# Optimization experiments

Hardware: AMD Instinct MI355X
Metric: run time of the kernel (lower is better)

Reference implementation:

```python
import jax, jax.numpy as jnp
import numpy as np

N_HEADS = 8
EMBED_C = 256  # key/query channels
OUT_C = 256    # value/output channels
MASK_CENTER = True

def setup_inputs() -> dict:
    key = jax.random.key(0)
    ks = jax.random.split(key, 5)
    B, C, H, W = 32, 256, 32, 32
    x = jax.random.normal(ks[0], (B, C, H, W), dtype=jnp.float32)
    # 1x1 conv weights as [out, in] matrices; scaled like torch conv default init
    s = 1.0 / np.sqrt(C)
    q_w = jax.random.normal(ks[1], (EMBED_C, C), dtype=jnp.float32) * s
    q_b = jax.random.normal(ks[2], (EMBED_C,), dtype=jnp.float32) * s
    kv_w = jax.random.normal(ks[3], (EMBED_C + OUT_C, C), dtype=jnp.float32) * s
    kv_b = jax.random.normal(ks[4], (EMBED_C + OUT_C,), dtype=jnp.float32) * s
    return {"x": x, "q_w": q_w, "q_b": q_b, "kv_w": kv_w, "kv_b": kv_b}

def _to_multihead(t):
    # t: (B, C, S) -> (B, n_heads, S, C // n_heads)
    B, C, S = t.shape
    return jnp.transpose(t.reshape(B, N_HEADS, C // N_HEADS, S), (0, 1, 3, 2))

def reference(x, q_w, q_b, kv_w, kv_b):
    B, C, H, W = x.shape
    S = H * W
    xf = x.reshape(B, C, S)  # flatten spatial; 1x1 conv == channel matmul
    q = jnp.einsum('oc,bcs->bos', q_w, xf) + q_b[None, :, None]
    kv = jnp.einsum('oc,bcs->bos', kv_w, xf) + kv_b[None, :, None]
    k, v = kv[:, :EMBED_C], kv[:, EMBED_C:]
    q = _to_multihead(q)   # (B, h, S, dk)
    k = _to_multihead(k)   # (B, h, S, dk)
    v = _to_multihead(v)   # (B, h, S, dv)
    dk = k.shape[-1]
    # strictly-lower-triangular causal mask (center pixel masked)
    mask = jnp.tril(jnp.ones((S, S), dtype=x.dtype), -int(MASK_CENTER))
    scores = jnp.einsum('bhqd,bhkd->bhqk', q, k) / jnp.sqrt(jnp.asarray(dk, x.dtype))
    scores = jnp.where(mask == 0, jnp.asarray(-10000.0, x.dtype), scores)
    attn = jax.nn.softmax(scores, axis=-1)
    attn = jnp.where(mask == 0, jnp.asarray(0.0, x.dtype), attn)
    out = jnp.einsum('bhqk,bhkd->bhqd', attn, v)  # (B, h, S, dv)
    out = jnp.transpose(out, (0, 1, 3, 2)).reshape(B, OUT_C, H, W)
    return out
```

## Files before the change

kernel.cpp:

```cpp
#include <hip/hip_runtime.h>
#include <hip/hip_bf16.h>

typedef __attribute__((ext_vector_type(8))) short short8;
typedef __attribute__((ext_vector_type(4))) float f32x4;
typedef __attribute__((ext_vector_type(16))) float f32x16;

#define B_  32
#define CH  256
#define S_  1024
#define NH  8
#define HD  32

static __device__ __forceinline__ unsigned short f2bf(float f) {
  __hip_bfloat16 h = __float2bfloat16(f);
  return *reinterpret_cast<unsigned short*>(&h);
}

static __device__ __forceinline__ void gl_lds16(const void* g, void* l) {
  __builtin_amdgcn_global_load_lds(
      (const __attribute__((address_space(1))) void*)g,
      (__attribute__((address_space(3))) void*)l, 16, 0, 0);
}

__global__ void k_prep(const float* __restrict__ x, unsigned short* __restrict__ xt,
                       const float* __restrict__ qw, const float* __restrict__ qb,
                       const float* __restrict__ kvw, const float* __restrict__ kvb,
                       unsigned short* __restrict__ wt, float* __restrict__ bias) {
  __shared__ float tile[32][33];
  int blk = (int)blockIdx.x;
  int t = threadIdx.x;
  if (blk < 8192) {
    int b = blk >> 8;
    int inner = blk & 255;
    int ct = inner >> 5, st = inner & 31;
    int c0 = ct * 32, s0 = st * 32;
    int r = t >> 3, q4 = (t & 7) * 4;
    const float4 v = *reinterpret_cast<const float4*>(
        x + ((size_t)(b * CH + c0 + r)) * S_ + s0 + q4);
    tile[r][q4 + 0] = v.x; tile[r][q4 + 1] = v.y;
    tile[r][q4 + 2] = v.z; tile[r][q4 + 3] = v.w;
    __syncthreads();
    ushort4 u;
    u.x = f2bf(tile[q4 + 0][r]); u.y = f2bf(tile[q4 + 1][r]);
    u.z = f2bf(tile[q4 + 2][r]); u.w = f2bf(tile[q4 + 3][r]);
    *reinterpret_cast<ushort4*>(xt + ((size_t)(b * S_ + s0 + r)) * CH + c0 + q4) = u;
  } else {
    int gid = (blk - 8192) * 256 + t;
    const float rs = 0.25503531838951954f;
    int o = gid >> 8, c = gid & 255;
    float v = (o < 256) ? qw[o * 256 + c] * rs : kvw[(o - 256) * 256 + c];
    wt[gid] = f2bf(v);
    if (gid < 768) bias[gid] = (gid < 256) ? qb[gid] * rs : kvb[gid - 256];
  }
}

__global__ __launch_bounds__(512) void k_proj(
    const unsigned short* __restrict__ wt, const float* __restrict__ bias,
    const unsigned short* __restrict__ xt,
    unsigned short* __restrict__ qws, unsigned short* __restrict__ kv) {
  __shared__ __align__(16) union {
    struct { unsigned short As[2][4096]; unsigned short Bs[2][4096]; } g;
    unsigned short vst[16384];
  } SH;
  int b = blockIdx.y;
  int mt = blockIdx.x >> 3, nt = blockIdx.x & 7;
  int tid = threadIdx.x;
  int wid = tid >> 6, l = tid & 63;
  int rb = l >> 4, lr = l & 15;
  int wr = wid >> 2, wc = wid & 3;
  int mb = mt * 128, nb = nt * 128;
  int wm = wr * 64, wn = wc * 32;
  const unsigned short* xb = xt + (size_t)b * S_ * CH;

  int r0 = tid >> 2, k0 = (tid & 3) * 8;
  const unsigned short* wa0 = wt + (size_t)(mb + r0) * CH + k0;
  const unsigned short* xb0 = xb + (size_t)(nb + r0) * CH + k0;
  char* asb = (char*)&SH.g.As[0][0];
  char* bsb = (char*)&SH.g.Bs[0][0];
  int wb = wid * 1024;

  f32x4 acc[4][2];
  #pragma unroll
  for (int mf = 0; mf < 4; ++mf)
    #pragma unroll
    for (int nf = 0; nf < 2; ++nf)
      acc[mf][nf] = (f32x4){0.f, 0.f, 0.f, 0.f};

  gl_lds16(wa0, asb + wb);
  gl_lds16(xb0, bsb + wb);
  __syncthreads();

  #pragma unroll 1
  for (int kk = 0; kk < 8; ++kk) {
    int cur = kk & 1;
    bool more = (kk < 7);
    if (more) {
      int ko = (kk + 1) * 32;
      int bo = (cur ^ 1) * 8192 + wb;
      gl_lds16(wa0 + ko, asb + bo);
      gl_lds16(xb0 + ko, bsb + bo);
    }

    short8 a[4], bfr[2];
    #pragma unroll
    for (int mf = 0; mf < 4; ++mf)
      a[mf] = *reinterpret_cast<const short8*>(
          &SH.g.As[cur][(wm + mf * 16 + lr) * 32 + rb * 8]);
    #pragma unroll
    for (int nf = 0; nf < 2; ++nf)
      bfr[nf] = *reinterpret_cast<const short8*>(
          &SH.g.Bs[cur][(wn + nf * 16 + lr) * 32 + rb * 8]);
    #pragma unroll
    for (int mf = 0; mf < 4; ++mf)
      #pragma unroll
      for (int nf = 0; nf < 2; ++nf)
        acc[mf][nf] = __builtin_amdgcn_mfma_f32_16x16x32_bf16(
            a[mf], bfr[nf], acc[mf][nf], 0, 0, 0);

    __syncthreads();
  }

  if (mb < 256) {
    #pragma unroll
    for (int mf = 0; mf < 4; ++mf) {
      int m0 = mb + wm + mf * 16 + rb * 4;
      const float4 bv = *reinterpret_cast<const float4*>(bias + m0);
      #pragma unroll
      for (int nf = 0; nf < 2; ++nf) {
        int n = nb + wn + nf * 16 + lr;
        ushort4 u = {f2bf(acc[mf][nf][0] + bv.x), f2bf(acc[mf][nf][1] + bv.y),
                     f2bf(acc[mf][nf][2] + bv.z), f2bf(acc[mf][nf][3] + bv.w)};
        int h = m0 >> 5, d = m0 & 31;
        *reinterpret_cast<ushort4*>(
            qws + ((size_t)(b * NH + h) * S_ + n) * HD + d) = u;
      }
    }
  } else {
    const bool isV = (mb >= 512);
    const int voff = isV ? 1024 : 0;
    unsigned short* vst = SH.vst;
    #pragma unroll
    for (int mf = 0; mf < 4; ++mf) {
      int m0 = mb + wm + mf * 16 + rb * 4;
      const float4 bv = *reinterpret_cast<const float4*>(bias + m0);
      int mml = wm + mf * 16 + rb * 4;
      int hl = mml >> 5, d0 = mml & 31;
      #pragma unroll
      for (int nf = 0; nf < 2; ++nf) {
        int nlc = wn + nf * 16 + lr;
        int tl = nlc >> 5, nl = nlc & 31;
        float v0 = acc[mf][nf][0] + bv.x;
        float v1 = acc[mf][nf][1] + bv.y;
        float v2 = acc[mf][nf][2] + bv.z;
        float v3 = acc[mf][nf][3] + bv.w;
        int tb = (hl * 4 + tl) * 1024;
        if (isV) {
          int kp = (nl & 19) | (((nl >> 2) & 1) << 3) | (((nl >> 3) & 1) << 2);
          int base = tb + (kp >> 3) * 256 + (kp & 7);
          vst[base + (size_t)(d0 + 0) * 8] = f2bf(v0);
          vst[base + (size_t)(d0 + 1) * 8] = f2bf(v1);
          vst[base + (size_t)(d0 + 2) * 8] = f2bf(v2);
          vst[base + (size_t)(d0 + 3) * 8] = f2bf(v3);
        } else {
          ushort4 u = {f2bf(v0), f2bf(v1), f2bf(v2), f2bf(v3)};
          *reinterpret_cast<ushort4*>(
              &vst[tb + (d0 >> 3) * 256 + nl * 8 + (d0 & 7)]) = u;
        }
      }
    }
    __syncthreads();
    int tt = tid >> 5, j = tid & 31;
    int hb = (isV ? (mb - 512) : (mb - 256)) >> 5;
    int h = hb + (tt >> 2);
    size_t gb = ((size_t)(b * NH + h) * 32 + (nt * 4 + (tt & 3))) * 2048 + voff;
    #pragma unroll
    for (int s = 0; s < 4; ++s) {
      int off = (j + s * 32) * 8;
      *reinterpret_cast<short8*>(kv + gb + off) =
          *reinterpret_cast<const short8*>(vst + tt * 1024 + off);
    }
  }
}

__global__ __launch_bounds__(512, 4) void k_attn(
    const unsigned short* __restrict__ qws, const unsigned short* __restrict__ kv,
    float* __restrict__ out) {
  __shared__ __align__(16) unsigned short kvbuf[2][8192];
  int tid = threadIdx.x;
  int wid = tid >> 6, l = tid & 63;
  int col = l & 31, hi = l >> 5;
  int bh = (int)(blockIdx.x & 255);
  int g  = 3 - (int)(blockIdx.x >> 8);
  int qt = g * 8 + wid;
  int q0 = qt << 5;
  int niter = g * 2 + 2;

  const unsigned short* Q   = qws + (size_t)bh * S_ * HD;
  const unsigned short* kvb = kv + (size_t)bh * 32 * 2048;
  char* kb0 = (char*)&kvbuf[0][0];
  int wb = wid * 1024;

  short8 aq0 = *reinterpret_cast<const short8*>(Q + (q0 + col) * HD + hi * 8);
  short8 aq1 = *reinterpret_cast<const short8*>(Q + (q0 + col) * HD + 16 + hi * 8);

  f32x16 z, O;
  #pragma unroll
  for (int i = 0; i < 16; ++i) { z[i] = 0.f; O[i] = 0.f; }
  float lsA = 0.f, lsB = 0.f;

  gl_lds16(kvb + tid * 8,        kb0 + wb);
  gl_lds16(kvb + 4096 + tid * 8, kb0 + 8192 + wb);
  __syncthreads();

  #pragma unroll 1
  for (int i = 0; i < niter; ++i) {
    int cur = i & 1;
    bool more = (i + 1 < niter);
    if (more) {
      const unsigned short* src = kvb + (size_t)(i + 1) * 8192 + tid * 8;
      char* dst = kb0 + (cur ^ 1) * 16384 + wb;
      gl_lds16(src,        dst);
      gl_lds16(src + 4096, dst + 8192);
    }

    #pragma unroll
    for (int sub = 0; sub < 4; ++sub) {
      int t = 4 * i + sub;
      if (qt >= t) {
        const unsigned short* Kb = &kvbuf[cur][sub * 2048];
        short8 bk0 = *reinterpret_cast<const short8*>(Kb + hi * 256 + col * 8);
        short8 bk1 = *reinterpret_cast<const short8*>(Kb + 512 + hi * 256 + col * 8);
        short8 av0 = *reinterpret_cast<const short8*>(Kb + 1024 + hi * 256 + col * 8);
        short8 av1 = *reinterpret_cast<const short8*>(Kb + 1536 + hi * 256 + col * 8);

        f32x16 st = __builtin_amdgcn_mfma_f32_32x32x16_bf16(bk0, aq0, z, 0, 0, 0);
        st = __builtin_amdgcn_mfma_f32_32x32x16_bf16(bk1, aq1, st, 0, 0, 0);

        float p[16];
        if (t == qt) {
          #pragma unroll
          for (int r = 0; r < 16; ++r) {
            int key = (r & 3) + 8 * (r >> 2) + 4 * hi;
            float e = __builtin_amdgcn_exp2f(st[r]);
            p[r] = (key < col) ? e : 0.f;
          }
        } else {
          #pragma unroll
          for (int r = 0; r < 16; ++r) p[r] = __builtin_amdgcn_exp2f(st[r]);
        }

        lsA += ((p[0] + p[1]) + (p[2] + p[3])) + ((p[4] + p[5]) + (p[6] + p[7]));
        lsB += ((p[8] + p[9]) + (p[10] + p[11])) + ((p[12] + p[13]) + (p[14] + p[15]));

        union { unsigned int u[8]; short8 v[2]; } pb;
        #pragma unroll
        for (int jj = 0; jj < 8; ++jj)
          asm("v_cvt_pk_bf16_f32 %0, %1, %2"
              : "=v"(pb.u[jj]) : "v"(p[2 * jj]), "v"(p[2 * jj + 1]));

        O = __builtin_amdgcn_mfma_f32_32x32x16_bf16(av0, pb.v[0], O, 0, 0, 0);
        O = __builtin_amdgcn_mfma_f32_32x32x16_bf16(av1, pb.v[1], O, 0, 0, 0);
      }
    }

    __syncthreads();
  }

  float lsum = lsA + lsB;
  float ltot = lsum + __shfl_xor(lsum, 32);
  float linv = (ltot > 0.f) ? 1.f / ltot : 0.f;
  int b = bh >> 3, h = bh & 7;
  float* ob = out + ((size_t)(b * 256 + h * 32)) * S_ + q0 + col;
  #pragma unroll
  for (int r = 0; r < 16; ++r) {
    int d = (r & 3) + 8 * (r >> 2) + 4 * hi;
    ob[(size_t)d * S_] = O[r] * linv;
  }
}

extern "C" void kernel_launch(void* const* d_in, const int* in_sizes, int n_in,
                              void* d_out, int out_size, void* d_ws, size_t ws_size,
                              hipStream_t stream) {
  const float* x   = (const float*)d_in[0];
  const float* qw  = (const float*)d_in[1];
  const float* qb  = (const float*)d_in[2];
  const float* kvw = (const float*)d_in[3];
  const float* kvb = (const float*)d_in[4];
  float* out = (float*)d_out;

  char* ws = (char*)d_ws;
  unsigned short* wt   = (unsigned short*)(ws + 0);
  float*          bias = (float*)(ws + 393216);
  unsigned short* xt   = (unsigned short*)(ws + 396288);
  unsigned short* qws  = (unsigned short*)(ws + 17173504);
  unsigned short* kv   = (unsigned short*)(ws + 33950720);

  k_prep<<<8960, 256, 0, stream>>>(x, xt, qw, qb, kvw, kvb, wt, bias);
  k_proj<<<dim3(48, 32), 512, 0, stream>>>(wt, bias, xt, qws, kv);
  k_attn<<<1024, 512, 0, stream>>>(qws, kv, out);
}
```

Before: 68.45 us.

## Triple-buffer projection GEMM with explicit vmcnt waits and one barrier per step

Replaces the double-buffered K loop in the projection kernel with a fully unrolled three-stage pipeline. Global-to-LDS loads are issued two steps ahead and gated with explicit s_waitcnt vmcnt counts, so each step needs one barrier instead of the trailing __syncthreads. A barrier is added before the epilogue reuses shared memory. This aims to hide global load latency in a short K loop, at the cost of more LDS and fragile hand-written wait and barrier ordering.

```diff
diff --git a/kernel.cpp b/kernel.cpp
--- a/kernel.cpp
+++ b/kernel.cpp
@@ -54,12 +54,43 @@
   }
 }
 
+
+#define VMW(n) asm volatile("s_waitcnt vmcnt(" #n ")" ::: "memory")
+#define SBAR() do { __builtin_amdgcn_s_barrier(); \
+                    __builtin_amdgcn_sched_barrier(0); } while (0)
+#define LGKM0() do { asm volatile("s_waitcnt lgkmcnt(0)" ::: "memory"); \
+                     __builtin_amdgcn_sched_barrier(0); } while (0)
+
+#define PROJ_ISSUE(step, buf) do {                                  \
+    gl_lds16(wa0 + (step) * 32, asb + (buf) * 8192 + wb);           \
+    gl_lds16(xb0 + (step) * 32, bsb + (buf) * 8192 + wb);           \
+  } while (0)
+
+#define PROJ_COMPUTE(buf) do {                                      \
+    short8 a[4], bfr[2];                                            \
+    _Pragma("unroll")                                               \
+    for (int mf = 0; mf < 4; ++mf)                                  \
+      a[mf] = *reinterpret_cast<const short8*>(                     \
+          &SH.g.As[buf][(wm + mf * 16 + lr) * 32 + rb * 8]);        \
+    _Pragma("unroll")                                               \
+    for (int nf = 0; nf < 2; ++nf)                                  \
+      bfr[nf] = *reinterpret_cast<const short8*>(                   \
+          &SH.g.Bs[buf][(wn + nf * 16 + lr) * 32 + rb * 8]);        \
+    LGKM0();                                                        \
+    _Pragma("unroll")                                               \
+    for (int mf = 0; mf < 4; ++mf)                                  \
+      _Pragma("unroll")                                             \
+      for (int nf = 0; nf < 2; ++nf)                                \
+        acc[mf][nf] = __builtin_amdgcn_mfma_f32_16x16x32_bf16(      \
+            a[mf], bfr[nf], acc[mf][nf], 0, 0, 0);                  \
+  } while (0)
+
 __global__ __launch_bounds__(512) void k_proj(
     const unsigned short* __restrict__ wt, const float* __restrict__ bias,
     const unsigned short* __restrict__ xt,
     unsigned short* __restrict__ qws, unsigned short* __restrict__ kv) {
   __shared__ __align__(16) union {
-    struct { unsigned short As[2][4096]; unsigned short Bs[2][4096]; } g;
+    struct { unsigned short As[3][4096]; unsigned short Bs[3][4096]; } g;
     unsigned short vst[16384];
   } SH;
   int b = blockIdx.y;
@@ -86,39 +117,16 @@
     for (int nf = 0; nf < 2; ++nf)
       acc[mf][nf] = (f32x4){0.f, 0.f, 0.f, 0.f};
 
-  gl_lds16(wa0, asb + wb);
-  gl_lds16(xb0, bsb + wb);
-  __syncthreads();
-
-  #pragma unroll 1
-  for (int kk = 0; kk < 8; ++kk) {
-    int cur = kk & 1;
-    bool more = (kk < 7);
-    if (more) {
-      int ko = (kk + 1) * 32;
-      int bo = (cur ^ 1) * 8192 + wb;
-      gl_lds16(wa0 + ko, asb + bo);
-      gl_lds16(xb0 + ko, bsb + bo);
-    }
-
-    short8 a[4], bfr[2];
-    #pragma unroll
-    for (int mf = 0; mf < 4; ++mf)
-      a[mf] = *reinterpret_cast<const short8*>(
-          &SH.g.As[cur][(wm + mf * 16 + lr) * 32 + rb * 8]);
-    #pragma unroll
-    for (int nf = 0; nf < 2; ++nf)
-      bfr[nf] = *reinterpret_cast<const short8*>(
-          &SH.g.Bs[cur][(wn + nf * 16 + lr) * 32 + rb * 8]);
-    #pragma unroll
-    for (int mf = 0; mf < 4; ++mf)
-      #pragma unroll
-      for (int nf = 0; nf < 2; ++nf)
-        acc[mf][nf] = __builtin_amdgcn_mfma_f32_16x16x32_bf16(
-            a[mf], bfr[nf], acc[mf][nf], 0, 0, 0);
-
-    __syncthreads();
-  }
+  PROJ_ISSUE(0, 0); PROJ_ISSUE(1, 1);
+
+  VMW(2); SBAR(); PROJ_ISSUE(2, 2); PROJ_COMPUTE(0);
+  VMW(2); SBAR(); PROJ_ISSUE(3, 0); PROJ_COMPUTE(1);
+  VMW(2); SBAR(); PROJ_ISSUE(4, 1); PROJ_COMPUTE(2);
+  VMW(2); SBAR(); PROJ_ISSUE(5, 2); PROJ_COMPUTE(0);
+  VMW(2); SBAR(); PROJ_ISSUE(6, 0); PROJ_COMPUTE(1);
+  VMW(2); SBAR(); PROJ_ISSUE(7, 1); PROJ_COMPUTE(2);
+  VMW(2); SBAR();                   PROJ_COMPUTE(0);
+  VMW(0); SBAR();                   PROJ_COMPUTE(1);
 
   if (mb < 256) {
     #pragma unroll
@@ -136,6 +144,7 @@
       }
     }
   } else {
+    __syncthreads();
     const bool isV = (mb >= 512);
     const int voff = isV ? 1024 : 0;
     unsigned short* vst = SH.vst;
```

New measurement: 67.84 us (median of 2 runs). No clear change (-0.9%).

## Fuse x transpose and bf16 conversion into projection GEMM loads

Applied to the files above, without the earlier changes.

Removes the separate pass that transposed x and converted it to bf16 in a workspace. The projection kernel now streams fp32 x tiles directly into LDS in channel-major layout and converts each element to bf16 while building the MFMA B fragments. This saves one full read and write of the activation tensor and a kernel launch. In exchange, global reads of x in the GEMM double in bytes, each tile is re-read by the six M-tiles, and B fragments are now built from scalar strided LDS reads plus per-element conversion.

```diff
diff --git a/kernel.cpp b/kernel.cpp
--- a/kernel.cpp
+++ b/kernel.cpp
@@ -22,44 +22,26 @@
       (__attribute__((address_space(3))) void*)l, 16, 0, 0);
 }
 
-__global__ void k_prep(const float* __restrict__ x, unsigned short* __restrict__ xt,
-                       const float* __restrict__ qw, const float* __restrict__ qb,
-                       const float* __restrict__ kvw, const float* __restrict__ kvb,
-                       unsigned short* __restrict__ wt, float* __restrict__ bias) {
-  __shared__ float tile[32][33];
-  int blk = (int)blockIdx.x;
-  int t = threadIdx.x;
-  if (blk < 8192) {
-    int b = blk >> 8;
-    int inner = blk & 255;
-    int ct = inner >> 5, st = inner & 31;
-    int c0 = ct * 32, s0 = st * 32;
-    int r = t >> 3, q4 = (t & 7) * 4;
-    const float4 v = *reinterpret_cast<const float4*>(
-        x + ((size_t)(b * CH + c0 + r)) * S_ + s0 + q4);
-    tile[r][q4 + 0] = v.x; tile[r][q4 + 1] = v.y;
-    tile[r][q4 + 2] = v.z; tile[r][q4 + 3] = v.w;
-    __syncthreads();
-    ushort4 u;
-    u.x = f2bf(tile[q4 + 0][r]); u.y = f2bf(tile[q4 + 1][r]);
-    u.z = f2bf(tile[q4 + 2][r]); u.w = f2bf(tile[q4 + 3][r]);
-    *reinterpret_cast<ushort4*>(xt + ((size_t)(b * S_ + s0 + r)) * CH + c0 + q4) = u;
-  } else {
-    int gid = (blk - 8192) * 256 + t;
-    const float rs = 0.25503531838951954f;
-    int o = gid >> 8, c = gid & 255;
-    float v = (o < 256) ? qw[o * 256 + c] * rs : kvw[(o - 256) * 256 + c];
-    wt[gid] = f2bf(v);
-    if (gid < 768) bias[gid] = (gid < 256) ? qb[gid] * rs : kvb[gid - 256];
-  }
+__global__ void k_wconv(const float* __restrict__ qw, const float* __restrict__ qb,
+                        const float* __restrict__ kvw, const float* __restrict__ kvb,
+                        unsigned short* __restrict__ wt, float* __restrict__ bias) {
+  int gid = (int)blockIdx.x * 256 + threadIdx.x;
+  const float rs = 0.25503531838951954f;
+  int o = gid >> 8, c = gid & 255;
+  float v = (o < 256) ? qw[o * 256 + c] * rs : kvw[(o - 256) * 256 + c];
+  wt[gid] = f2bf(v);
+  if (gid < 768) bias[gid] = (gid < 256) ? qb[gid] * rs : kvb[gid - 256];
 }
 
 __global__ __launch_bounds__(512) void k_proj(
     const unsigned short* __restrict__ wt, const float* __restrict__ bias,
-    const unsigned short* __restrict__ xt,
+    const float* __restrict__ x,
     unsigned short* __restrict__ qws, unsigned short* __restrict__ kv) {
   __shared__ __align__(16) union {
-    struct { unsigned short As[2][4096]; unsigned short Bs[2][4096]; } g;
+    struct {
+      unsigned short As[2][4096];
+      float Bf[2][4096];
+    } g;
     unsigned short vst[16384];
   } SH;
   int b = blockIdx.y;
@@ -70,13 +52,12 @@
   int wr = wid >> 2, wc = wid & 3;
   int mb = mt * 128, nb = nt * 128;
   int wm = wr * 64, wn = wc * 32;
-  const unsigned short* xb = xt + (size_t)b * S_ * CH;
-
-  int r0 = tid >> 2, k0 = (tid & 3) * 8;
-  const unsigned short* wa0 = wt + (size_t)(mb + r0) * CH + k0;
-  const unsigned short* xb0 = xb + (size_t)(nb + r0) * CH + k0;
+
+  const unsigned short* wa0 = wt + (size_t)(mb + (tid >> 2)) * CH + (tid & 3) * 8;
+  const float* xsrc = x + (size_t)b * CH * S_
+                    + (size_t)(tid >> 5) * S_ + nb + (tid & 31) * 4;
   char* asb = (char*)&SH.g.As[0][0];
-  char* bsb = (char*)&SH.g.Bs[0][0];
+  char* bfb = (char*)&SH.g.Bf[0][0];
   int wb = wid * 1024;
 
   f32x4 acc[4][2];
@@ -87,18 +68,19 @@
       acc[mf][nf] = (f32x4){0.f, 0.f, 0.f, 0.f};
 
   gl_lds16(wa0, asb + wb);
-  gl_lds16(xb0, bsb + wb);
+  gl_lds16(xsrc,             bfb + wb);
+  gl_lds16(xsrc + 16 * S_,   bfb + 8192 + wb);
   __syncthreads();
 
   #pragma unroll 1
   for (int kk = 0; kk < 8; ++kk) {
     int cur = kk & 1;
-    bool more = (kk < 7);
-    if (more) {
+    if (kk < 7) {
       int ko = (kk + 1) * 32;
-      int bo = (cur ^ 1) * 8192 + wb;
-      gl_lds16(wa0 + ko, asb + bo);
-      gl_lds16(xb0 + ko, bsb + bo);
+      gl_lds16(wa0 + ko, asb + (cur ^ 1) * 8192 + wb);
+      const float* xs = xsrc + (size_t)ko * S_;
+      gl_lds16(xs,           bfb + (cur ^ 1) * 16384 + wb);
+      gl_lds16(xs + 16 * S_, bfb + (cur ^ 1) * 16384 + 8192 + wb);
     }
 
     short8 a[4], bfr[2];
@@ -107,9 +89,12 @@
       a[mf] = *reinterpret_cast<const short8*>(
           &SH.g.As[cur][(wm + mf * 16 + lr) * 32 + rb * 8]);
     #pragma unroll
-    for (int nf = 0; nf < 2; ++nf)
-      bfr[nf] = *reinterpret_cast<const short8*>(
-          &SH.g.Bs[cur][(wn + nf * 16 + lr) * 32 + rb * 8]);
+    for (int nf = 0; nf < 2; ++nf) {
+      int nn = wn + nf * 16 + lr;
+      #pragma unroll
+      for (int j = 0; j < 8; ++j)
+        bfr[nf][j] = (short)f2bf(SH.g.Bf[cur][(rb * 8 + j) * 128 + nn]);
+    }
     #pragma unroll
     for (int mf = 0; mf < 4; ++mf)
       #pragma unroll
@@ -291,11 +276,10 @@
   char* ws = (char*)d_ws;
   unsigned short* wt   = (unsigned short*)(ws + 0);
   float*          bias = (float*)(ws + 393216);
-  unsigned short* xt   = (unsigned short*)(ws + 396288);
   unsigned short* qws  = (unsigned short*)(ws + 17173504);
   unsigned short* kv   = (unsigned short*)(ws + 33950720);
 
-  k_prep<<<8960, 256, 0, stream>>>(x, xt, qw, qb, kvw, kvb, wt, bias);
-  k_proj<<<dim3(48, 32), 512, 0, stream>>>(wt, bias, xt, qws, kv);
+  k_wconv<<<768, 256, 0, stream>>>(qw, qb, kvw, kvb, wt, bias);
+  k_proj<<<dim3(48, 32), 512, 0, stream>>>(wt, bias, x, qws, kv);
   k_attn<<<1024, 512, 0, stream>>>(qws, kv, out);
 }
```

New measurement: 69.89 us. +2.1%, slower.
